# Kernel optimization log

Hardware: AMD Instinct MI355X
Metric: run time of the kernel (lower is better)

The kernel has to match this reference:

```python
import jax, jax.numpy as jnp
import numpy as np

H = 256        # hidden_size
NC = 15        # num_components (decode steps)
V = 26         # vocab_size
E = 64         # embed_dim
B = 65536      # batch


def setup_inputs() -> dict:
    key = jax.random.key(0)
    ks = jax.random.split(key, 8)
    return {
        "context": jax.random.normal(ks[0], (B, H), jnp.float32),
        "embed_table": (jax.random.normal(ks[1], (V, E), jnp.float32) * 0.02),
        "start_embed": (jax.random.normal(ks[2], (E,), jnp.float32) * 0.02),
        "Wp": jax.random.normal(ks[3], (H, H), jnp.float32) / np.sqrt(H),
        "bp": jnp.zeros((H,), jnp.float32),
        "Wi": jax.random.normal(ks[4], (H + E, 4 * H), jnp.float32) / np.sqrt(H + E),
        "Wh": jax.random.normal(ks[5], (H, 4 * H), jnp.float32) / np.sqrt(H),
        "bh": jnp.zeros((4 * H,), jnp.float32),
        "Wo": jax.random.normal(ks[6], (H, V), jnp.float32) / np.sqrt(H),
        "bo": jnp.zeros((V,), jnp.float32),
        "seed": 0,
    }


def _lstm_step(c, h, x, Wi, Wh, bh):
    # flax OptimizedLSTMCell: fused gates, order i, f, g, o; bias on hidden path only
    gates = x @ Wi + h @ Wh + bh            # (B, 4H)
    i, f, g, o = jnp.split(gates, 4, axis=-1)
    c_new = jax.nn.sigmoid(f) * c + jax.nn.sigmoid(i) * jnp.tanh(g)
    h_new = jax.nn.sigmoid(o) * jnp.tanh(c_new)
    return c_new, h_new


def reference(context, embed_table, start_embed, Wp, bp, Wi, Wh, bh, Wo, bo, seed):
    b = context.shape[0]
    h = jnp.tanh(context @ Wp + bp)          # init_proj + tanh
    c = jnp.zeros_like(h)
    prev = jnp.broadcast_to(start_embed, (b, start_embed.shape[0]))
    keys = jax.random.split(jax.random.key(seed), NC)  # one subkey per decode step

    def step(carry, k):
        c, h, prev = carry
        x = jnp.concatenate([context, prev], axis=-1)   # (B, H+E)
        c, h = _lstm_step(c, h, x, Wi, Wh, bh)
        logits = h @ Wo + bo                            # (B, V)
        tok = jax.random.categorical(k, logits, axis=-1)  # (B,) int
        prev = embed_table[tok]                         # embedding lookup
        return (c, h, prev), (logits, tok)

    _, (logits, samples) = jax.lax.scan(step, (c, h, prev), keys)
    # scan stacks on axis 0 (time); move to (B, NC, ...)
    return jnp.transpose(logits, (1, 0, 2)), jnp.transpose(samples, (1, 0))
```

## Files before the change

### kernel.cpp

```cpp
#include <hip/hip_runtime.h>
#include <cstdint>
#include <cstddef>

#define NROWS 16
#define NTHR  256
#define HSZ   256
#define ESZ   64
#define VSZ   26
#define NCOMP 15
#define BATCH 65536

#define JAX_PARTITIONABLE 1

__device__ __forceinline__ uint32_t rotl32(uint32_t v, int d) {
  return (v << d) | (v >> (32 - d));
}

__device__ __forceinline__ void tf2x32(uint32_t kA, uint32_t kB,
                                       uint32_t& x0, uint32_t& x1) {
  uint32_t kC = kA ^ kB ^ 0x1BD11BDAu;
  x0 += kA; x1 += kB;
#define TFR(r) { x0 += x1; x1 = rotl32(x1, r); x1 ^= x0; }
  TFR(13) TFR(15) TFR(26) TFR(6)
  x0 += kB; x1 += kC + 1u;
  TFR(17) TFR(29) TFR(16) TFR(24)
  x0 += kC; x1 += kA + 2u;
  TFR(13) TFR(15) TFR(26) TFR(6)
  x0 += kA; x1 += kB + 3u;
  TFR(17) TFR(29) TFR(16) TFR(24)
  x0 += kB; x1 += kC + 4u;
  TFR(13) TFR(15) TFR(26) TFR(6)
  x0 += kC; x1 += kA + 5u;
#undef TFR
}

__device__ __forceinline__ float xla_tanh(float x) {
  #pragma clang fp contract(off)
  float ax = fabsf(x);
  float xc = fminf(fmaxf(x, -7.90531110763549805f), 7.90531110763549805f);
  float x2 = xc * xc;
  float nu = -2.76076847742355e-16f;
  nu = x2 * nu + 2.00018790482477e-13f;
  nu = x2 * nu + -8.60467152213735e-11f;
  nu = x2 * nu + 5.12229709037114e-08f;
  nu = x2 * nu + 1.48572235717979e-05f;
  nu = x2 * nu + 6.37261928875436e-04f;
  nu = x2 * nu + 4.89352455891786e-03f;
  nu = xc * nu;
  float de = 1.19825839466702e-06f;
  de = x2 * de + 1.18534705686654e-04f;
  de = x2 * de + 2.26843463243900e-03f;
  de = x2 * de + 4.89352518554385e-03f;
  float r = nu / de;
  return (ax < 0.0004f) ? x : r;
}

__device__ __forceinline__ float xla_sigmoid(float x) {
  #pragma clang fp contract(off)
  return 0.5f + 0.5f * xla_tanh(0.5f * x);
}

__device__ __forceinline__ float xla_log(float x) {
  #pragma clang fp contract(off)
  uint32_t bits = __float_as_uint(x);
  int ei = (int)(bits >> 23) - 126;
  float m = __uint_as_float((bits & 0x007FFFFFu) | 0x3F000000u);
  bool lt = m < 0.707106781186547524f;
  float ee = (float)ei - (lt ? 1.0f : 0.0f);
  float mm = (m - 1.0f) + (lt ? m : 0.0f);
  float x2 = mm * mm;
  float x3 = x2 * mm;
  float y  = __builtin_fmaf(7.0376836292E-2f,  mm, -1.1514610310E-1f);
  float y1 = __builtin_fmaf(-1.2420140846E-1f, mm,  1.4249322787E-1f);
  float y2 = __builtin_fmaf(2.0000714765E-1f,  mm, -2.4999993993E-1f);
  y  = __builtin_fmaf(y,  mm, 1.1676998740E-1f);
  y1 = __builtin_fmaf(y1, mm, -1.6668057665E-1f);
  y2 = __builtin_fmaf(y2, mm, 3.3333331174E-1f);
  y  = __builtin_fmaf(y, x3, y1);
  y  = __builtin_fmaf(y, x3, y2);
  y  = y * x3;
  float t1 = ee * -2.12194440e-4f;
  float t2 = 0.5f * x2;
  y  = y + t1;
  mm = mm - t2;
  float t3 = ee * 0.693359375f;
  mm = mm + y;
  mm = mm + t3;
  return mm;
}

__device__ __forceinline__ void chain4(float* aI, float* aF, float* aG, float* aO,
                                       const float* lds, const float* W, int u, int nk) {
  const float* w = W + u;
  for (int k = 0; k < nk; ++k) {
    float wI = w[0], wF = w[256], wG = w[512], wO = w[768];
    w += 1024;
    float hv[16];
    *(float4*)&hv[0]  = *(const float4*)(lds + k * 16 + 0);
    *(float4*)&hv[4]  = *(const float4*)(lds + k * 16 + 4);
    *(float4*)&hv[8]  = *(const float4*)(lds + k * 16 + 8);
    *(float4*)&hv[12] = *(const float4*)(lds + k * 16 + 12);
    #pragma unroll
    for (int r = 0; r < 16; ++r) {
      aI[r] = __builtin_fmaf(hv[r], wI, aI[r]);
      aF[r] = __builtin_fmaf(hv[r], wF, aF[r]);
      aG[r] = __builtin_fmaf(hv[r], wG, aG[r]);
      aO[r] = __builtin_fmaf(hv[r], wO, aO[r]);
    }
  }
}

__global__ __launch_bounds__(NTHR, 2) void belief_main(
    const float* __restrict__ ctx, const float* __restrict__ embed,
    const float* __restrict__ start_e, const float* __restrict__ Wp,
    const float* __restrict__ bp, const float* __restrict__ Wi,
    const float* __restrict__ Wh, const float* __restrict__ bh,
    const float* __restrict__ Wo, const float* __restrict__ bo,
    const int* __restrict__ seedp, float* __restrict__ out,
    float* __restrict__ ctxG, int fast) {
  __shared__ __align__(16) float hT[HSZ * NROWS];
  __shared__ __align__(16) float ctxT[HSZ * NROWS];
  __shared__ __align__(16) float prevT[ESZ * NROWS];
  __shared__ __align__(16) float woLds[HSZ * VSZ];
  __shared__ float boLds[VSZ];
  __shared__ float scores[NROWS * VSZ];
  __shared__ int tokLds[NROWS];
  __shared__ uint32_t skLds[NCOMP * 2];

  const int t = threadIdx.x;
  const int b0 = blockIdx.x * NROWS;

  #pragma unroll
  for (int r = 0; r < NROWS; ++r)
    ctxT[t * NROWS + r] = ctx[(size_t)(b0 + r) * HSZ + t];
  for (int i = t; i < HSZ * VSZ; i += NTHR) woLds[i] = Wo[i];
  if (t < VSZ) boLds[t] = bo[t];
  for (int i = t; i < ESZ * NROWS; i += NTHR) prevT[i] = start_e[i >> 4];
  if (t < NCOMP) {
    uint32_t x0, x1;
#if JAX_PARTITIONABLE
    x0 = 0u; x1 = (uint32_t)t;
    tf2x32(0u, (uint32_t)seedp[0], x0, x1);
    skLds[2 * t] = x0; skLds[2 * t + 1] = x1;
#else
    {
      uint32_t idx0 = (uint32_t)(2 * t), idx1 = (uint32_t)(2 * t + 1);
      uint32_t a, b;
      if (idx0 < 15u) { a = idx0; b = idx0 + 15u; tf2x32(0u, (uint32_t)seedp[0], a, b); skLds[2*t] = a; }
      else            { a = idx0 - 15u; b = idx0; tf2x32(0u, (uint32_t)seedp[0], a, b); skLds[2*t] = b; }
      if (idx1 < 15u) { a = idx1; b = idx1 + 15u; tf2x32(0u, (uint32_t)seedp[0], a, b); skLds[2*t+1] = a; }
      else            { a = idx1 - 15u; b = idx1; tf2x32(0u, (uint32_t)seedp[0], a, b); skLds[2*t+1] = b; }
    }
#endif
  }
  __syncthreads();

  float c[NROWS];
  {
    float acc[NROWS];
    #pragma unroll
    for (int r = 0; r < NROWS; ++r) acc[r] = 0.0f;
    const float* wp = Wp + t;
    for (int m = 0; m < HSZ; ++m) {
      float w = wp[(size_t)m * HSZ];
      float hv[16];
      *(float4*)&hv[0]  = *(const float4*)&ctxT[m * NROWS + 0];
      *(float4*)&hv[4]  = *(const float4*)&ctxT[m * NROWS + 4];
      *(float4*)&hv[8]  = *(const float4*)&ctxT[m * NROWS + 8];
      *(float4*)&hv[12] = *(const float4*)&ctxT[m * NROWS + 12];
      #pragma unroll
      for (int r = 0; r < NROWS; ++r) acc[r] = __builtin_fmaf(hv[r], w, acc[r]);
    }
    float bpv = bp[t];
    #pragma unroll
    for (int r = 0; r < NROWS; ++r) {
      float s = acc[r] + bpv;
      hT[t * NROWS + r] = xla_tanh(s);
      c[r] = 0.0f;
    }
  }

  if (fast) {
    float aI[16], aF[16], aG[16], aO[16];
    #pragma unroll
    for (int r = 0; r < 16; ++r) { aI[r] = 0.f; aF[r] = 0.f; aG[r] = 0.f; aO[r] = 0.f; }
    chain4(aI, aF, aG, aO, ctxT, Wi, t, HSZ);
    #pragma unroll
    for (int r = 0; r < 16; ++r) {
      size_t base = (size_t)(b0 + r) * 1024 + t;
      ctxG[base] = aI[r]; ctxG[base + 256] = aF[r];
      ctxG[base + 512] = aG[r]; ctxG[base + 768] = aO[r];
    }
  }
  __syncthreads();

  const float bhI = bh[t], bhF = bh[256 + t], bhG = bh[512 + t], bhO = bh[768 + t];
  const float* WiP = Wi + (size_t)HSZ * 1024;

  for (int s = 0; s < NCOMP; ++s) {
    float aI[16], aF[16], aG[16], aO[16];
    if (fast) {
      #pragma unroll
      for (int r = 0; r < 16; ++r) {
        size_t base = (size_t)(b0 + r) * 1024 + t;
        aI[r] = ctxG[base]; aF[r] = ctxG[base + 256];
        aG[r] = ctxG[base + 512]; aO[r] = ctxG[base + 768];
      }
    } else {
      #pragma unroll
      for (int r = 0; r < 16; ++r) { aI[r] = 0.f; aF[r] = 0.f; aG[r] = 0.f; aO[r] = 0.f; }
      chain4(aI, aF, aG, aO, ctxT, Wi, t, HSZ);
    }
    chain4(aI, aF, aG, aO, prevT, WiP, t, ESZ);

    float bI[16], bF[16], bG[16], bO[16];
    #pragma unroll
    for (int r = 0; r < 16; ++r) { bI[r] = 0.f; bF[r] = 0.f; bG[r] = 0.f; bO[r] = 0.f; }
    chain4(bI, bF, bG, bO, hT, Wh, t, HSZ);

    float hnew[16];
    {
      #pragma clang fp contract(off)
      #pragma unroll
      for (int r = 0; r < 16; ++r) {
        float gi = (aI[r] + bI[r]) + bhI;
        float gf = (aF[r] + bF[r]) + bhF;
        float gg = (aG[r] + bG[r]) + bhG;
        float go = (aO[r] + bO[r]) + bhO;
        float si = xla_sigmoid(gi);
        float sf = xla_sigmoid(gf);
        float tg = xla_tanh(gg);
        float so = xla_sigmoid(go);
        float cn = sf * c[r] + si * tg;
        c[r] = cn;
        hnew[r] = so * xla_tanh(cn);
      }
    }
    __syncthreads();
    #pragma unroll
    for (int r = 0; r < 16; ++r) hT[t * NROWS + r] = hnew[r];
    __syncthreads();

    uint32_t sk0 = skLds[2 * s], sk1 = skLds[2 * s + 1];
    for (int p = t; p < NROWS * VSZ; p += NTHR) {
      int r = p / VSZ, v = p - r * VSZ;
      float acc = 0.0f;
      for (int k = 0; k < HSZ; ++k)
        acc = __builtin_fmaf(hT[k * NROWS + r], woLds[k * VSZ + v], acc);
      float logit = acc + boLds[v];
      out[(size_t)(b0 + r) * (NCOMP * VSZ) + s * VSZ + v] = logit;

      uint32_t n = (uint32_t)(b0 + r) * VSZ + (uint32_t)v;
      uint32_t x0, x1, rb;
#if JAX_PARTITIONABLE
      x0 = 0u; x1 = n;
      tf2x32(sk0, sk1, x0, x1);
      rb = x0 ^ x1;
#else
      {
        const uint32_t half = (uint32_t)(BATCH * VSZ / 2);
        if (n < half) { x0 = n; x1 = n + half; tf2x32(sk0, sk1, x0, x1); rb = x0; }
        else          { x0 = n - half; x1 = n; tf2x32(sk0, sk1, x0, x1); rb = x1; }
      }
#endif
      float f = __uint_as_float((rb >> 9) | 0x3F800000u) - 1.0f;
      float uu;
      {
        #pragma clang fp contract(off)
        uu = f + 1.17549435082228751e-38f;
      }
      uu = fmaxf(1.17549435082228751e-38f, uu);
      float l1 = xla_log(uu);
      float g = -xla_log(-l1);
      {
        #pragma clang fp contract(off)
        scores[r * VSZ + v] = g + logit;
      }
    }
    __syncthreads();

    if (t < NROWS) {
      float mbest = scores[t * VSZ];
      int ibest = 0;
      for (int v = 1; v < VSZ; ++v) {
        float sc = scores[t * VSZ + v];
        if (sc > mbest) { mbest = sc; ibest = v; }
      }
      tokLds[t] = ibest;
      out[(size_t)BATCH * (NCOMP * VSZ) + (size_t)(b0 + t) * NCOMP + s] = (float)ibest;
    }
    __syncthreads();
    if (s < NCOMP - 1) {
      for (int i = t; i < ESZ * NROWS; i += NTHR) {
        int e = i >> 4, r = i & 15;
        prevT[i] = embed[tokLds[r] * ESZ + e];
      }
    }
    __syncthreads();
  }
}

extern "C" void kernel_launch(void* const* d_in, const int* in_sizes, int n_in,
                              void* d_out, int out_size, void* d_ws, size_t ws_size,
                              hipStream_t stream) {
  const float* ctx     = (const float*)d_in[0];
  const float* embed   = (const float*)d_in[1];
  const float* start_e = (const float*)d_in[2];
  const float* Wp      = (const float*)d_in[3];
  const float* bp      = (const float*)d_in[4];
  const float* Wi      = (const float*)d_in[5];
  const float* Wh      = (const float*)d_in[6];
  const float* bh      = (const float*)d_in[7];
  const float* Wo      = (const float*)d_in[8];
  const float* bo      = (const float*)d_in[9];
  const int*   seedp   = (const int*)d_in[10];
  float* out = (float*)d_out;

  size_t need = (size_t)BATCH * 1024 * sizeof(float);
  int fast = (d_ws != nullptr && ws_size >= need) ? 1 : 0;
  float* ctxG = (float*)d_ws;

  hipLaunchKernelGGL(belief_main, dim3(BATCH / NROWS), dim3(NTHR), 0, stream,
                     ctx, embed, start_e, Wp, bp, Wi, Wh, bh, Wo, bo, seedp,
                     out, ctxG, fast);
}
```

Measured before the change: 10.02 ms.

## Repack LSTM gate weights into float4 and keep context projection in registers

Adds a small pre-kernel that interleaves the four gate columns of Wi and Wh into float4 so each k-step does one vector load instead of four scalar loads. Replaces the global-memory ctxG cache of the context gate projection with a per-thread register copy (pI..pO, 64 extra floats) reused across all steps. The register copy removes about 256MB of workspace traffic per step but raises register pressure, which under launch_bounds(256,2) may cause spills. It also drops the unused non-partitionable RNG branch.

```diff
diff --git a/kernel.cpp b/kernel.cpp
--- a/kernel.cpp
+++ b/kernel.cpp
@@ -9,8 +9,6 @@
 #define VSZ   26
 #define NCOMP 15
 #define BATCH 65536
-
-#define JAX_PARTITIONABLE 1
 
 __device__ __forceinline__ uint32_t rotl32(uint32_t v, int d) {
   return (v << d) | (v >> (32 - d));
@@ -95,18 +93,50 @@
   for (int k = 0; k < nk; ++k) {
     float wI = w[0], wF = w[256], wG = w[512], wO = w[768];
     w += 1024;
-    float hv[16];
-    *(float4*)&hv[0]  = *(const float4*)(lds + k * 16 + 0);
-    *(float4*)&hv[4]  = *(const float4*)(lds + k * 16 + 4);
-    *(float4*)&hv[8]  = *(const float4*)(lds + k * 16 + 8);
-    *(float4*)&hv[12] = *(const float4*)(lds + k * 16 + 12);
-    #pragma unroll
-    for (int r = 0; r < 16; ++r) {
-      aI[r] = __builtin_fmaf(hv[r], wI, aI[r]);
-      aF[r] = __builtin_fmaf(hv[r], wF, aF[r]);
-      aG[r] = __builtin_fmaf(hv[r], wG, aG[r]);
-      aO[r] = __builtin_fmaf(hv[r], wO, aO[r]);
-    }
+    #pragma unroll
+    for (int rq = 0; rq < 4; ++rq) {
+      float hv[4];
+      *(float4*)hv = *(const float4*)(lds + k * 16 + rq * 4);
+      #pragma unroll
+      for (int j = 0; j < 4; ++j) {
+        int r = rq * 4 + j;
+        aI[r] = __builtin_fmaf(hv[j], wI, aI[r]);
+        aF[r] = __builtin_fmaf(hv[j], wF, aF[r]);
+        aG[r] = __builtin_fmaf(hv[j], wG, aG[r]);
+        aO[r] = __builtin_fmaf(hv[j], wO, aO[r]);
+      }
+    }
+  }
+}
+
+__device__ __forceinline__ void chain4v(float* aI, float* aF, float* aG, float* aO,
+                                        const float* lds, const float4* W4, int u, int nk) {
+  const float4* w = W4 + u;
+  #pragma unroll 2
+  for (int k = 0; k < nk; ++k) {
+    float4 wv = w[(size_t)k * 256];
+    #pragma unroll
+    for (int rq = 0; rq < 4; ++rq) {
+      float hv[4];
+      *(float4*)hv = *(const float4*)(lds + k * 16 + rq * 4);
+      #pragma unroll
+      for (int j = 0; j < 4; ++j) {
+        int r = rq * 4 + j;
+        aI[r] = __builtin_fmaf(hv[j], wv.x, aI[r]);
+        aF[r] = __builtin_fmaf(hv[j], wv.y, aF[r]);
+        aG[r] = __builtin_fmaf(hv[j], wv.z, aG[r]);
+        aO[r] = __builtin_fmaf(hv[j], wv.w, aO[r]);
+      }
+    }
+  }
+}
+
+__global__ void repack_w(const float* __restrict__ W, float4* __restrict__ W4, int n) {
+  int i = blockIdx.x * blockDim.x + threadIdx.x;
+  if (i < n) {
+    int k = i >> 8, u = i & 255;
+    const float* src = W + (size_t)k * 1024 + u;
+    W4[i] = make_float4(src[0], src[256], src[512], src[768]);
   }
 }
 
@@ -117,7 +147,7 @@
     const float* __restrict__ Wh, const float* __restrict__ bh,
     const float* __restrict__ Wo, const float* __restrict__ bo,
     const int* __restrict__ seedp, float* __restrict__ out,
-    float* __restrict__ ctxG, int fast) {
+    const float4* __restrict__ Wi4, const float4* __restrict__ Wh4, int packed) {
   __shared__ __align__(16) float hT[HSZ * NROWS];
   __shared__ __align__(16) float ctxT[HSZ * NROWS];
   __shared__ __align__(16) float prevT[ESZ * NROWS];
@@ -137,21 +167,9 @@
   if (t < VSZ) boLds[t] = bo[t];
   for (int i = t; i < ESZ * NROWS; i += NTHR) prevT[i] = start_e[i >> 4];
   if (t < NCOMP) {
-    uint32_t x0, x1;
-#if JAX_PARTITIONABLE
-    x0 = 0u; x1 = (uint32_t)t;
+    uint32_t x0 = 0u, x1 = (uint32_t)t;
     tf2x32(0u, (uint32_t)seedp[0], x0, x1);
     skLds[2 * t] = x0; skLds[2 * t + 1] = x1;
-#else
-    {
-      uint32_t idx0 = (uint32_t)(2 * t), idx1 = (uint32_t)(2 * t + 1);
-      uint32_t a, b;
-      if (idx0 < 15u) { a = idx0; b = idx0 + 15u; tf2x32(0u, (uint32_t)seedp[0], a, b); skLds[2*t] = a; }
-      else            { a = idx0 - 15u; b = idx0; tf2x32(0u, (uint32_t)seedp[0], a, b); skLds[2*t] = b; }
-      if (idx1 < 15u) { a = idx1; b = idx1 + 15u; tf2x32(0u, (uint32_t)seedp[0], a, b); skLds[2*t+1] = a; }
-      else            { a = idx1 - 15u; b = idx1; tf2x32(0u, (uint32_t)seedp[0], a, b); skLds[2*t+1] = b; }
-    }
-#endif
   }
   __syncthreads();
 
@@ -163,13 +181,14 @@
     const float* wp = Wp + t;
     for (int m = 0; m < HSZ; ++m) {
       float w = wp[(size_t)m * HSZ];
-      float hv[16];
-      *(float4*)&hv[0]  = *(const float4*)&ctxT[m * NROWS + 0];
-      *(float4*)&hv[4]  = *(const float4*)&ctxT[m * NROWS + 4];
-      *(float4*)&hv[8]  = *(const float4*)&ctxT[m * NROWS + 8];
-      *(float4*)&hv[12] = *(const float4*)&ctxT[m * NROWS + 12];
       #pragma unroll
-      for (int r = 0; r < NROWS; ++r) acc[r] = __builtin_fmaf(hv[r], w, acc[r]);
+      for (int rq = 0; rq < 4; ++rq) {
+        float hv[4];
+        *(float4*)hv = *(const float4*)&ctxT[m * NROWS + rq * 4];
+        #pragma unroll
+        for (int j = 0; j < 4; ++j)
+          acc[rq * 4 + j] = __builtin_fmaf(hv[j], w, acc[rq * 4 + j]);
+      }
     }
     float bpv = bp[t];
     #pragma unroll
@@ -180,43 +199,29 @@
     }
   }
 
-  if (fast) {
-    float aI[16], aF[16], aG[16], aO[16];
-    #pragma unroll
-    for (int r = 0; r < 16; ++r) { aI[r] = 0.f; aF[r] = 0.f; aG[r] = 0.f; aO[r] = 0.f; }
-    chain4(aI, aF, aG, aO, ctxT, Wi, t, HSZ);
-    #pragma unroll
-    for (int r = 0; r < 16; ++r) {
-      size_t base = (size_t)(b0 + r) * 1024 + t;
-      ctxG[base] = aI[r]; ctxG[base + 256] = aF[r];
-      ctxG[base + 512] = aG[r]; ctxG[base + 768] = aO[r];
-    }
-  }
+  float pI[16], pF[16], pG[16], pO[16];
+  #pragma unroll
+  for (int r = 0; r < 16; ++r) { pI[r] = 0.f; pF[r] = 0.f; pG[r] = 0.f; pO[r] = 0.f; }
+  if (packed) chain4v(pI, pF, pG, pO, ctxT, Wi4, t, HSZ);
+  else        chain4 (pI, pF, pG, pO, ctxT, Wi,  t, HSZ);
   __syncthreads();
 
   const float bhI = bh[t], bhF = bh[256 + t], bhG = bh[512 + t], bhO = bh[768 + t];
-  const float* WiP = Wi + (size_t)HSZ * 1024;
+  const float*  WiP  = Wi  + (size_t)HSZ * 1024;
+  const float4* WiP4 = Wi4 + (size_t)HSZ * 256;
 
   for (int s = 0; s < NCOMP; ++s) {
     float aI[16], aF[16], aG[16], aO[16];
-    if (fast) {
-      #pragma unroll
-      for (int r = 0; r < 16; ++r) {
-        size_t base = (size_t)(b0 + r) * 1024 + t;
-        aI[r] = ctxG[base]; aF[r] = ctxG[base + 256];
-        aG[r] = ctxG[base + 512]; aO[r] = ctxG[base + 768];
-      }
-    } else {
-      #pragma unroll
-      for (int r = 0; r < 16; ++r) { aI[r] = 0.f; aF[r] = 0.f; aG[r] = 0.f; aO[r] = 0.f; }
-      chain4(aI, aF, aG, aO, ctxT, Wi, t, HSZ);
-    }
-    chain4(aI, aF, aG, aO, prevT, WiP, t, ESZ);
+    #pragma unroll
+    for (int r = 0; r < 16; ++r) { aI[r] = pI[r]; aF[r] = pF[r]; aG[r] = pG[r]; aO[r] = pO[r]; }
+    if (packed) chain4v(aI, aF, aG, aO, prevT, WiP4, t, ESZ);
+    else        chain4 (aI, aF, aG, aO, prevT, WiP,  t, ESZ);
 
     float bI[16], bF[16], bG[16], bO[16];
     #pragma unroll
     for (int r = 0; r < 16; ++r) { bI[r] = 0.f; bF[r] = 0.f; bG[r] = 0.f; bO[r] = 0.f; }
-    chain4(bI, bF, bG, bO, hT, Wh, t, HSZ);
+    if (packed) chain4v(bI, bF, bG, bO, hT, Wh4, t, HSZ);
+    else        chain4 (bI, bF, bG, bO, hT, Wh,  t, HSZ);
 
     float hnew[16];
     {
@@ -251,18 +256,9 @@
       out[(size_t)(b0 + r) * (NCOMP * VSZ) + s * VSZ + v] = logit;
 
       uint32_t n = (uint32_t)(b0 + r) * VSZ + (uint32_t)v;
-      uint32_t x0, x1, rb;
-#if JAX_PARTITIONABLE
-      x0 = 0u; x1 = n;
+      uint32_t x0 = 0u, x1 = n;
       tf2x32(sk0, sk1, x0, x1);
-      rb = x0 ^ x1;
-#else
-      {
-        const uint32_t half = (uint32_t)(BATCH * VSZ / 2);
-        if (n < half) { x0 = n; x1 = n + half; tf2x32(sk0, sk1, x0, x1); rb = x0; }
-        else          { x0 = n - half; x1 = n; tf2x32(sk0, sk1, x0, x1); rb = x1; }
-      }
-#endif
+      uint32_t rb = x0 ^ x1;
       float f = __uint_as_float((rb >> 9) | 0x3F800000u) - 1.0f;
       float uu;
       {
@@ -316,11 +312,20 @@
   const int*   seedp   = (const int*)d_in[10];
   float* out = (float*)d_out;
 
-  size_t need = (size_t)BATCH * 1024 * sizeof(float);
-  int fast = (d_ws != nullptr && ws_size >= need) ? 1 : 0;
-  float* ctxG = (float*)d_ws;
+  size_t wi4_elems = (size_t)(HSZ + ESZ) * 256;
+  size_t wh4_elems = (size_t)HSZ * 256;
+  size_t need = (wi4_elems + wh4_elems) * sizeof(float4);
+  int packed = (d_ws != nullptr && ws_size >= need) ? 1 : 0;
+  float4* Wi4 = (float4*)d_ws;
+  float4* Wh4 = Wi4 + wi4_elems;
+
+  if (packed) {
+    int nWi = (int)wi4_elems, nWh = (int)wh4_elems;
+    hipLaunchKernelGGL(repack_w, dim3((nWi + 255) / 256), dim3(256), 0, stream, Wi, Wi4, nWi);
+    hipLaunchKernelGGL(repack_w, dim3((nWh + 255) / 256), dim3(256), 0, stream, Wh, Wh4, nWh);
+  }
 
   hipLaunchKernelGGL(belief_main, dim3(BATCH / NROWS), dim3(NTHR), 0, stream,
                      ctx, embed, start_e, Wp, bp, Wi, Wh, bh, Wo, bo, seedp,
-                     out, ctxG, fast);
-}
+                     out, Wi4, Wh4, packed);
+}
```

After: 10.52 ms. +5.0%, slower.
